# Kernel tuning notes

Measured on AMD Instinct MI355X. Metric: run time of the kernel, lower is better.

The kernel has to match this reference:

```python
import jax, jax.numpy as jnp
import numpy as np

NUM_USERS = 100000
NUM_ITEMS = 50000
EMB_DIM = 64
USER_FEAT = 256
ITEM_FEAT = 256
NUM_EDGES = 1000000
NUM_LAYERS = 4
N = NUM_USERS + NUM_ITEMS


def setup_inputs() -> dict:
    key = jax.random.key(0)
    ks = jax.random.split(key, 8)
    edge_index = jax.random.randint(ks[0], (2, NUM_EDGES), 0, N, dtype=jnp.int64 if jax.config.x64_enabled else jnp.int32).astype(jnp.int32)
    emb_users = jax.random.normal(ks[1], (NUM_USERS, EMB_DIM), dtype=jnp.float32) * 0.1
    emb_items = jax.random.normal(ks[2], (NUM_ITEMS, EMB_DIM), dtype=jnp.float32) * 0.1
    users_features = jax.random.normal(ks[3], (NUM_USERS, USER_FEAT), dtype=jnp.float32)
    items_features = jax.random.normal(ks[4], (NUM_ITEMS, ITEM_FEAT), dtype=jnp.float32)
    # original init is zeros; use small random weights for a non-trivial baseline
    user_proj_w = jax.random.normal(ks[5], (EMB_DIM, USER_FEAT), dtype=jnp.float32) * 0.01
    item_proj_w = jax.random.normal(ks[6], (EMB_DIM, ITEM_FEAT), dtype=jnp.float32) * 0.01
    return {
        "edge_index": edge_index,
        "emb_users": emb_users,
        "emb_items": emb_items,
        "users_features": users_features,
        "items_features": items_features,
        "user_proj_w": user_proj_w,
        "item_proj_w": item_proj_w,
    }


def reference(edge_index, emb_users, emb_items, users_features, items_features, user_proj_w, item_proj_w):
    row, col = edge_index[0], edge_index[1]
    # symmetric GCN normalization without self-loops (PyG LGConv)
    deg = jax.ops.segment_sum(jnp.ones_like(col, dtype=emb_users.dtype), col, num_segments=N)
    dinv = jnp.where(deg > 0, jax.lax.rsqrt(jnp.maximum(deg, 1.0)), 0.0)
    norm = dinv[row] * dinv[col]  # [E]

    x = jnp.concatenate([emb_users, emb_items], axis=0)  # [N, D]
    acc = x
    for _ in range(NUM_LAYERS):
        msgs = x[row] * norm[:, None]                      # [E, D] gather + scale
        x = jax.ops.segment_sum(msgs, col, num_segments=N)  # scatter-add
        acc = acc + x
    # mean over (L+1) layer embeddings, then extra 1/(L+1) factor (faithful to source)
    emb_final = acc / ((NUM_LAYERS + 1) ** 2)

    u_final = emb_final[:NUM_USERS] + users_features @ user_proj_w.T
    i_final = emb_final[NUM_USERS:] + items_features @ item_proj_w.T
    return (u_final, i_final)
```

## Files before the change

### kernel.cpp

```cpp
#include <hip/hip_runtime.h>

#define U_NODES 100000
#define I_NODES 50000
#define N_NODES 150000
#define EMB_D   64
#define FEAT_K  256
#define N_LAYERS 4

typedef __attribute__((ext_vector_type(8))) short short8;
typedef __attribute__((ext_vector_type(4))) float f32x4;

static __device__ __forceinline__ unsigned short f2bf(float f) {
    unsigned u = __builtin_bit_cast(unsigned, f);
    u += 0x7fffu + ((u >> 16) & 1u);
    return (unsigned short)(u >> 16);
}
static __device__ __forceinline__ float bflo(unsigned u) {
    return __builtin_bit_cast(float, u << 16);
}
static __device__ __forceinline__ float bfhi(unsigned u) {
    return __builtin_bit_cast(float, u & 0xffff0000u);
}

__global__ __launch_bounds__(256) void k_count(const int* __restrict__ col,
                                               int* __restrict__ deg, int E) {
    int e = blockIdx.x * 256 + threadIdx.x;
    if (e < E) atomicAdd(&deg[col[e]], 1);
}

__global__ __launch_bounds__(256) void k_dinv(const int* __restrict__ deg,
                                              float* __restrict__ dinv, int n) {
    int i = blockIdx.x * 256 + threadIdx.x;
    if (i < n) {
        int d = deg[i];
        dinv[i] = (d > 0) ? rsqrtf((float)d) : 0.0f;
    }
}

__global__ __launch_bounds__(256) void k_scan_a(const int* __restrict__ deg,
                                                int* __restrict__ rs,
                                                int* __restrict__ bsum, int n) {
    __shared__ int wsum[4];
    int t = threadIdx.x;
    int i = blockIdx.x * 256 + t;
    int v = (i < n) ? deg[i] : 0;
    int x = v;
    #pragma unroll
    for (int off = 1; off < 64; off <<= 1) {
        int y = __shfl_up(x, off, 64);
        if ((t & 63) >= off) x += y;
    }
    if ((t & 63) == 63) wsum[t >> 6] = x;
    __syncthreads();
    int base = 0;
    #pragma unroll
    for (int w = 0; w < 4; ++w) base += (w < (t >> 6)) ? wsum[w] : 0;
    if (i < n) rs[i] = base + x - v;
    if (t == 255) bsum[blockIdx.x] = base + x;
}

__global__ __launch_bounds__(1024) void k_scan_b(int* __restrict__ bs, int nb) {
    __shared__ int wsum[16];
    int t = threadIdx.x;
    int v = (t < nb) ? bs[t] : 0;
    int x = v;
    #pragma unroll
    for (int off = 1; off < 64; off <<= 1) {
        int y = __shfl_up(x, off, 64);
        if ((t & 63) >= off) x += y;
    }
    if ((t & 63) == 63) wsum[t >> 6] = x;
    __syncthreads();
    int base = 0;
    #pragma unroll
    for (int w = 0; w < 16; ++w) base += (w < (t >> 6)) ? wsum[w] : 0;
    if (t < nb) bs[t] = base + x - v;
}

__global__ __launch_bounds__(256) void k_scan_c(int* __restrict__ rs,
                                                const int* __restrict__ bsum,
                                                int* __restrict__ cursor,
                                                int n, int E) {
    int i = blockIdx.x * 256 + threadIdx.x;
    if (i < n) {
        int v = rs[i] + bsum[blockIdx.x];
        rs[i] = v;
        cursor[i] = v;
    }
    if (i == 0) rs[n] = E;
}

__global__ __launch_bounds__(256) void k_fill(const int* __restrict__ row,
                                              const int* __restrict__ col,
                                              const float* __restrict__ dinv,
                                              int* __restrict__ cursor,
                                              int2* __restrict__ csr, int E) {
    int e = blockIdx.x * 256 + threadIdx.x;
    if (e < E) {
        int r = row[e], c = col[e];
        int p = atomicAdd(&cursor[c], 1);
        int2 v;
        v.x = r;
        v.y = __builtin_bit_cast(int, dinv[r] * dinv[c]);
        csr[p] = v;
    }
}

__global__ __launch_bounds__(256) void k_cvtw(const float* __restrict__ wu,
                                              const float* __restrict__ wi,
                                              unsigned short* __restrict__ wub,
                                              unsigned short* __restrict__ wib) {
    int i = blockIdx.x * 256 + threadIdx.x;
    if (i < EMB_D * FEAT_K) wub[i] = f2bf(wu[i]);
    else                    wib[i - EMB_D * FEAT_K] = f2bf(wi[i - EMB_D * FEAT_K]);
}

__global__ __launch_bounds__(256) void k_init(const float4* __restrict__ eu,
                                              const float4* __restrict__ ei,
                                              uint4* __restrict__ x,
                                              int n8u, int n8) {
    int i = blockIdx.x * 256 + threadIdx.x;
    if (i >= n8) return;
    const float4* s = (i < n8u) ? (eu + (size_t)i * 2) : (ei + (size_t)(i - n8u) * 2);
    float4 p0 = s[0], p1 = s[1];
    uint4 r;
    r.x = (unsigned)f2bf(p0.x) | ((unsigned)f2bf(p0.y) << 16);
    r.y = (unsigned)f2bf(p0.z) | ((unsigned)f2bf(p0.w) << 16);
    r.z = (unsigned)f2bf(p1.x) | ((unsigned)f2bf(p1.y) << 16);
    r.w = (unsigned)f2bf(p1.z) | ((unsigned)f2bf(p1.w) << 16);
    x[i] = r;
}

#define ACC8(v_, w_)                       \
    s0 = fmaf(bflo((v_).x), (w_), s0);     \
    s1 = fmaf(bfhi((v_).x), (w_), s1);     \
    s2 = fmaf(bflo((v_).y), (w_), s2);     \
    s3 = fmaf(bfhi((v_).y), (w_), s3);     \
    s4 = fmaf(bflo((v_).z), (w_), s4);     \
    s5 = fmaf(bfhi((v_).z), (w_), s5);     \
    s6 = fmaf(bflo((v_).w), (w_), s6);     \
    s7 = fmaf(bfhi((v_).w), (w_), s7);

#define GATHER4(xsrc_, ep_, em_)                                              \
    {                                                                         \
        int i0_ = (ep_), i1_ = min((ep_) + 1, (em_));                         \
        int i2_ = min((ep_) + 2, (em_)), i3_ = min((ep_) + 3, (em_));         \
        int2 pa_ = csr[i0_], pb_ = csr[i1_], pc_ = csr[i2_], pd_ = csr[i3_];  \
        float wa_ = __builtin_bit_cast(float, pa_.y);                         \
        float wb_ = ((ep_) + 1 <= (em_)) ? __builtin_bit_cast(float, pb_.y) : 0.f; \
        float wc_ = ((ep_) + 2 <= (em_)) ? __builtin_bit_cast(float, pc_.y) : 0.f; \
        float wd_ = ((ep_) + 3 <= (em_)) ? __builtin_bit_cast(float, pd_.y) : 0.f; \
        uint4 va_ = (xsrc_)[(size_t)pa_.x * 8 + lane];                        \
        uint4 vb_ = (xsrc_)[(size_t)pb_.x * 8 + lane];                        \
        uint4 vc_ = (xsrc_)[(size_t)pc_.x * 8 + lane];                        \
        uint4 vd_ = (xsrc_)[(size_t)pd_.x * 8 + lane];                        \
        ACC8(va_, wa_) ACC8(vb_, wb_) ACC8(vc_, wc_) ACC8(vd_, wd_)           \
    }

__global__ __launch_bounds__(256) void k_agg(const uint4* __restrict__ xin,
                                             uint4* __restrict__ xout,
                                             const int* __restrict__ rs,
                                             const int2* __restrict__ csr,
                                             int n_nodes) {
    int idx = blockIdx.x * 256 + threadIdx.x;
    int node = idx >> 3;
    int lane = idx & 7;
    if (node >= n_nodes) return;
    int e0 = rs[node], e1 = rs[node + 1];
    float s0 = 0.f, s1 = 0.f, s2 = 0.f, s3 = 0.f;
    float s4 = 0.f, s5 = 0.f, s6 = 0.f, s7 = 0.f;
    int em = e1 - 1;
    for (int ep = e0; ep < e1; ep += 4) GATHER4(xin, ep, em)
    uint4 r;
    r.x = (unsigned)f2bf(s0) | ((unsigned)f2bf(s1) << 16);
    r.y = (unsigned)f2bf(s2) | ((unsigned)f2bf(s3) << 16);
    r.z = (unsigned)f2bf(s4) | ((unsigned)f2bf(s5) << 16);
    r.w = (unsigned)f2bf(s6) | ((unsigned)f2bf(s7) << 16);
    xout[(size_t)node * 8 + lane] = r;
}

__global__ __launch_bounds__(256) void k_agg4(const uint4* __restrict__ x3,
                                              const uint4* __restrict__ x1,
                                              const uint4* __restrict__ x2,
                                              const float* __restrict__ embU,
                                              const float* __restrict__ embI,
                                              float* __restrict__ outp,
                                              const int* __restrict__ rs,
                                              const int2* __restrict__ csr,
                                              int n_nodes, int U) {
    int idx = blockIdx.x * 256 + threadIdx.x;
    int node = idx >> 3;
    int lane = idx & 7;
    if (node >= n_nodes) return;
    int e0 = rs[node], e1 = rs[node + 1];
    float s0 = 0.f, s1 = 0.f, s2 = 0.f, s3 = 0.f;
    float s4 = 0.f, s5 = 0.f, s6 = 0.f, s7 = 0.f;
    int em = e1 - 1;
    for (int ep = e0; ep < e1; ep += 4) GATHER4(x3, ep, em)
    uint4 v1 = x1[(size_t)node * 8 + lane];
    uint4 v2 = x2[(size_t)node * 8 + lane];
    uint4 v3 = x3[(size_t)node * 8 + lane];
    const float* ebp = (node < U) ? (embU + (size_t)node * EMB_D)
                                  : (embI + (size_t)(node - U) * EMB_D);
    float4 ea = ((const float4*)ebp)[lane * 2];
    float4 eb2 = ((const float4*)ebp)[lane * 2 + 1];
    const float sc = 1.0f / 25.0f;
    float4 o0, o1;
    o0.x = (ea.x  + bflo(v1.x) + bflo(v2.x) + bflo(v3.x) + s0) * sc;
    o0.y = (ea.y  + bfhi(v1.x) + bfhi(v2.x) + bfhi(v3.x) + s1) * sc;
    o0.z = (ea.z  + bflo(v1.y) + bflo(v2.y) + bflo(v3.y) + s2) * sc;
    o0.w = (ea.w  + bfhi(v1.y) + bfhi(v2.y) + bfhi(v3.y) + s3) * sc;
    o1.x = (eb2.x + bflo(v1.z) + bflo(v2.z) + bflo(v3.z) + s4) * sc;
    o1.y = (eb2.y + bfhi(v1.z) + bfhi(v2.z) + bfhi(v3.z) + s5) * sc;
    o1.z = (eb2.z + bflo(v1.w) + bflo(v2.w) + bflo(v3.w) + s6) * sc;
    o1.w = (eb2.w + bfhi(v1.w) + bfhi(v2.w) + bfhi(v3.w) + s7) * sc;
    float4* op = (float4*)(outp + (size_t)node * EMB_D) + lane * 2;
    op[0] = o0;
    op[1] = o1;
}

__global__ __launch_bounds__(256) void k_projm(const float* __restrict__ FU,
                                               const float* __restrict__ FI,
                                               const unsigned short* __restrict__ WUb,
                                               const unsigned short* __restrict__ WIb,
                                               float* __restrict__ out,
                                               int nbU, int U, int I) {
    __shared__ float sA[16 * 256];
    const bool isU = ((int)blockIdx.x < nbU);
    const float* __restrict__ F = isU ? FU : FI;
    const uint4* __restrict__ Wb4 = (const uint4*)(isU ? WUb : WIb);
    float* __restrict__ o = isU ? out : out + (size_t)U * EMB_D;
    const int M = isU ? U : I;
    const int tile = isU ? (int)blockIdx.x : (int)blockIdx.x - nbU;
    const int row0 = tile * 16;
    const int wave = threadIdx.x >> 6;
    const int lane = threadIdx.x & 63;
    const int l15  = lane & 15;
    const int kq   = lane >> 4;

    const uint4* wp = Wb4 + (size_t)(wave * 16 + l15) * 32 + kq;
    uint4 B0 = wp[0],  B1 = wp[4],  B2 = wp[8],  B3 = wp[12];
    uint4 B4 = wp[16], B5 = wp[20], B6 = wp[24], B7 = wp[28];

    #pragma unroll
    for (int j = 0; j < 4; ++j) {
        int r = wave * 4 + j;
        int grow = min(row0 + r, M - 1);
        int sboff = (lane * 16) ^ ((r & 7) << 4);
        const float* src = F + (size_t)grow * FEAT_K + (sboff >> 2);
        __builtin_amdgcn_global_load_lds(
            (const __attribute__((address_space(1))) void*)src,
            (__attribute__((address_space(3))) void*)(sA + r * 256),
            16, 0, 0);
    }
    __syncthreads();

    f32x4 acc = {0.f, 0.f, 0.f, 0.f};
    const char* arow_p = (const char*)(sA + l15 * 256);
    const int sw = (l15 & 7) << 4;

#define CVT2(d_, lo_, hi_) asm("v_cvt_pk_bf16_f32 %0, %1, %2" : "=v"(d_) : "v"(lo_), "v"(hi_))
#define KS(ks_, B_)                                                            \
    {                                                                          \
        int cb = (ks_) * 128 + kq * 32;                                        \
        f32x4 lo = *(const f32x4*)(arow_p + ((cb) ^ sw));                      \
        f32x4 hi = *(const f32x4*)(arow_p + ((cb + 16) ^ sw));                 \
        unsigned p0, p1, p2, p3;                                               \
        CVT2(p0, lo[0], lo[1]); CVT2(p1, lo[2], lo[3]);                        \
        CVT2(p2, hi[0], hi[1]); CVT2(p3, hi[2], hi[3]);                        \
        uint4 up; up.x = p0; up.y = p1; up.z = p2; up.w = p3;                  \
        short8 av = __builtin_bit_cast(short8, up);                            \
        short8 bv = __builtin_bit_cast(short8, B_);                            \
        acc = __builtin_amdgcn_mfma_f32_16x16x32_bf16(av, bv, acc, 0, 0, 0);   \
    }

    KS(0, B0) KS(1, B1) KS(2, B2) KS(3, B3)
    KS(4, B4) KS(5, B5) KS(6, B6) KS(7, B7)
#undef KS
#undef CVT2

    #pragma unroll
    for (int r = 0; r < 4; ++r) {
        int grow = row0 + kq * 4 + r;
        if (grow < M) {
            float* op = o + (size_t)grow * EMB_D + wave * 16 + l15;
            op[0] += acc[r];
        }
    }
}

extern "C" void kernel_launch(void* const* d_in, const int* in_sizes, int n_in,
                              void* d_out, int out_size, void* d_ws, size_t ws_size,
                              hipStream_t stream) {
    const int E = in_sizes[0] / 2;
    const int N = N_NODES, U = U_NODES;

    const int*   edge  = (const int*)d_in[0];
    const float* emb_u = (const float*)d_in[1];
    const float* emb_i = (const float*)d_in[2];
    const float* fu    = (const float*)d_in[3];
    const float* fi    = (const float*)d_in[4];
    const float* wu    = (const float*)d_in[5];
    const float* wi    = (const float*)d_in[6];
    const int* row = edge;
    const int* col = edge + E;

    const int NB  = (N + 255) / 256;
    const int EB  = (E + 255) / 256;
    const int XB8 = ((N * 8) + 255) / 256;

    char* p = (char*)d_ws;
    auto carve = [&](size_t bytes) -> void* {
        void* q = (void*)p;
        p += (bytes + 255) & ~(size_t)255;
        return q;
    };
    float* dinv    = (float*)carve((size_t)N * 4);
    int*   deg     = (int*)  carve((size_t)N * 4);
    int*   rs      = (int*)  carve((size_t)(N + 1) * 4);
    int*   cursor  = (int*)  carve((size_t)N * 4);
    int*   bsum    = (int*)  carve(1024 * 4);
    int2*  csr     = (int2*) carve((size_t)E * 8);
    unsigned short* wub = (unsigned short*)carve((size_t)EMB_D * FEAT_K * 2);
    unsigned short* wib = (unsigned short*)carve((size_t)EMB_D * FEAT_K * 2);
    uint4* x0 = (uint4*)carve((size_t)N * EMB_D * 2);
    uint4* x1 = (uint4*)carve((size_t)N * EMB_D * 2);
    uint4* x2 = (uint4*)carve((size_t)N * EMB_D * 2);
    uint4* x3 = (uint4*)carve((size_t)N * EMB_D * 2);

    float* outp = (float*)d_out;

    hipMemsetAsync(deg, 0, (size_t)N * 4, stream);
    k_count<<<EB, 256, 0, stream>>>(col, deg, E);
    k_dinv<<<NB, 256, 0, stream>>>(deg, dinv, N);
    k_scan_a<<<NB, 256, 0, stream>>>(deg, rs, bsum, N);
    k_scan_b<<<1, 1024, 0, stream>>>(bsum, NB);
    k_scan_c<<<NB, 256, 0, stream>>>(rs, bsum, cursor, N, E);
    k_fill<<<EB, 256, 0, stream>>>(row, col, dinv, cursor, csr, E);
    k_cvtw<<<(2 * EMB_D * FEAT_K) / 256, 256, 0, stream>>>(wu, wi, wub, wib);
    k_init<<<XB8, 256, 0, stream>>>((const float4*)emb_u, (const float4*)emb_i,
                                    x0, U * 8, N * 8);
    k_agg<<<XB8, 256, 0, stream>>>(x0, x1, rs, csr, N);
    k_agg<<<XB8, 256, 0, stream>>>(x1, x2, rs, csr, N);
    k_agg<<<XB8, 256, 0, stream>>>(x2, x3, rs, csr, N);
    k_agg4<<<XB8, 256, 0, stream>>>(x3, x1, x2, emb_u, emb_i, outp, rs, csr, N, U);
    const int nbU = (U + 15) / 16;
    const int nbI = (N - U + 15) / 16;
    k_projm<<<nbU + nbI, 256, 0, stream>>>(fu, fi, wub, wib, outp, nbU, U, N - U);
}
```

Before: 280.8 us.

## Make projection GEMM persistent with double-buffered LDS prefetch; batch k_fill edges

The projection kernel becomes persistent with a fixed grid of 1280 blocks. Each block loops over 16-row tiles and prefetches the next tile's features into a second LDS buffer while the current one runs through MFMA, so global-to-LDS latency overlaps compute. Weights stay in registers and are reloaded only when the loop crosses from the user range into the item range. Separately, k_fill now handles four edges per thread with vectorised int4 loads of row and col, exposing more independent atomics per thread. The cost is manual waitcnt and barrier management, which is fragile, and fewer resident blocks.

```diff
diff --git a/kernel.cpp b/kernel.cpp
--- a/kernel.cpp
+++ b/kernel.cpp
@@ -95,14 +95,30 @@
                                               const float* __restrict__ dinv,
                                               int* __restrict__ cursor,
                                               int2* __restrict__ csr, int E) {
-    int e = blockIdx.x * 256 + threadIdx.x;
-    if (e < E) {
-        int r = row[e], c = col[e];
-        int p = atomicAdd(&cursor[c], 1);
-        int2 v;
-        v.x = r;
-        v.y = __builtin_bit_cast(int, dinv[r] * dinv[c]);
-        csr[p] = v;
+    int base = (blockIdx.x * 256 + threadIdx.x) * 4;
+    if (base >= E) return;
+    if (base + 4 <= E) {
+        int4 c4 = *(const int4*)(col + base);
+        int4 r4 = *(const int4*)(row + base);
+        float na = dinv[r4.x] * dinv[c4.x];
+        float nb = dinv[r4.y] * dinv[c4.y];
+        float nc = dinv[r4.z] * dinv[c4.z];
+        float nd = dinv[r4.w] * dinv[c4.w];
+        int pa = atomicAdd(&cursor[c4.x], 1);
+        int pb = atomicAdd(&cursor[c4.y], 1);
+        int pc = atomicAdd(&cursor[c4.z], 1);
+        int pd = atomicAdd(&cursor[c4.w], 1);
+        int2 va; va.x = r4.x; va.y = __builtin_bit_cast(int, na); csr[pa] = va;
+        int2 vb; vb.x = r4.y; vb.y = __builtin_bit_cast(int, nb); csr[pb] = vb;
+        int2 vc; vc.x = r4.z; vc.y = __builtin_bit_cast(int, nc); csr[pc] = vc;
+        int2 vd; vd.x = r4.w; vd.y = __builtin_bit_cast(int, nd); csr[pd] = vd;
+    } else {
+        for (int e = base; e < E; ++e) {
+            int r = row[e], c = col[e];
+            int p = atomicAdd(&cursor[c], 1);
+            int2 v; v.x = r; v.y = __builtin_bit_cast(int, dinv[r] * dinv[c]);
+            csr[p] = v;
+        }
     }
 }
 
@@ -219,52 +235,88 @@
     op[1] = o1;
 }
 
+#define PROJ_GRID 1280
+
+__device__ __forceinline__ void proj_stage(const float* __restrict__ FU,
+                                           const float* __restrict__ FI,
+                                           int nbU, int U, int I, int t,
+                                           float* dst, int wave, int lane) {
+    bool su = t < nbU;
+    const float* F = su ? FU : FI;
+    int tl = su ? t : t - nbU;
+    int M  = su ? U : I;
+    int r0 = tl * 16;
+    #pragma unroll
+    for (int j = 0; j < 4; ++j) {
+        int r = wave * 4 + j;
+        int g = min(r0 + r, M - 1);
+        int sb = (lane * 16) ^ ((r & 7) << 4);
+        const float* src = F + (size_t)g * FEAT_K + (sb >> 2);
+        __builtin_amdgcn_global_load_lds(
+            (const __attribute__((address_space(1))) void*)src,
+            (__attribute__((address_space(3))) void*)(dst + r * 256),
+            16, 0, 0);
+    }
+}
+
 __global__ __launch_bounds__(256) void k_projm(const float* __restrict__ FU,
                                                const float* __restrict__ FI,
                                                const unsigned short* __restrict__ WUb,
                                                const unsigned short* __restrict__ WIb,
                                                float* __restrict__ out,
-                                               int nbU, int U, int I) {
-    __shared__ float sA[16 * 256];
-    const bool isU = ((int)blockIdx.x < nbU);
-    const float* __restrict__ F = isU ? FU : FI;
-    const uint4* __restrict__ Wb4 = (const uint4*)(isU ? WUb : WIb);
-    float* __restrict__ o = isU ? out : out + (size_t)U * EMB_D;
-    const int M = isU ? U : I;
-    const int tile = isU ? (int)blockIdx.x : (int)blockIdx.x - nbU;
-    const int row0 = tile * 16;
+                                               int nbU, int U, int I, int nT) {
+    __shared__ float sA[2][16 * 256];
     const int wave = threadIdx.x >> 6;
     const int lane = threadIdx.x & 63;
     const int l15  = lane & 15;
     const int kq   = lane >> 4;
-
-    const uint4* wp = Wb4 + (size_t)(wave * 16 + l15) * 32 + kq;
+    const int sw   = (l15 & 7) << 4;
+
+    int t = blockIdx.x;
+    proj_stage(FU, FI, nbU, U, I, t, sA[0], wave, lane);
+    bool curU = (t < nbU);
+    const uint4* wp = (curU ? (const uint4*)WUb : (const uint4*)WIb)
+                      + (size_t)(wave * 16 + l15) * 32 + kq;
     uint4 B0 = wp[0],  B1 = wp[4],  B2 = wp[8],  B3 = wp[12];
     uint4 B4 = wp[16], B5 = wp[20], B6 = wp[24], B7 = wp[28];
 
-    #pragma unroll
-    for (int j = 0; j < 4; ++j) {
-        int r = wave * 4 + j;
-        int grow = min(row0 + r, M - 1);
-        int sboff = (lane * 16) ^ ((r & 7) << 4);
-        const float* src = F + (size_t)grow * FEAT_K + (sboff >> 2);
-        __builtin_amdgcn_global_load_lds(
-            (const __attribute__((address_space(1))) void*)src,
-            (__attribute__((address_space(3))) void*)(sA + r * 256),
-            16, 0, 0);
-    }
-    __syncthreads();
-
-    f32x4 acc = {0.f, 0.f, 0.f, 0.f};
-    const char* arow_p = (const char*)(sA + l15 * 256);
-    const int sw = (l15 & 7) << 4;
+    int buf = 0;
+    for (; t < nT; t += PROJ_GRID) {
+        int tn = t + PROJ_GRID;
+        if (tn < nT) {
+            proj_stage(FU, FI, nbU, U, I, tn, sA[buf ^ 1], wave, lane);
+            asm volatile("s_waitcnt vmcnt(4)" ::: "memory");
+        } else {
+            asm volatile("s_waitcnt vmcnt(0)" ::: "memory");
+        }
+        __builtin_amdgcn_sched_barrier(0);
+        __builtin_amdgcn_s_barrier();
+        __builtin_amdgcn_sched_barrier(0);
+
+        bool u = (t < nbU);
+        if (u != curU) {
+            const uint4* wq = (u ? (const uint4*)WUb : (const uint4*)WIb)
+                              + (size_t)(wave * 16 + l15) * 32 + kq;
+            B0 = wq[0];  B1 = wq[4];  B2 = wq[8];  B3 = wq[12];
+            B4 = wq[16]; B5 = wq[20]; B6 = wq[24]; B7 = wq[28];
+            curU = u;
+        }
+
+        {
+            bool su = u;
+            float* o = su ? out : out + (size_t)U * EMB_D;
+            int tl = su ? t : t - nbU;
+            int M  = su ? U : I;
+            int r0 = tl * 16;
+            f32x4 acc = {0.f, 0.f, 0.f, 0.f};
+            const char* ap = (const char*)(sA[buf] + l15 * 256);
 
 #define CVT2(d_, lo_, hi_) asm("v_cvt_pk_bf16_f32 %0, %1, %2" : "=v"(d_) : "v"(lo_), "v"(hi_))
 #define KS(ks_, B_)                                                            \
     {                                                                          \
         int cb = (ks_) * 128 + kq * 32;                                        \
-        f32x4 lo = *(const f32x4*)(arow_p + ((cb) ^ sw));                      \
-        f32x4 hi = *(const f32x4*)(arow_p + ((cb + 16) ^ sw));                 \
+        f32x4 lo = *(const f32x4*)(ap + ((cb) ^ sw));                          \
+        f32x4 hi = *(const f32x4*)(ap + ((cb + 16) ^ sw));                     \
         unsigned p0, p1, p2, p3;                                               \
         CVT2(p0, lo[0], lo[1]); CVT2(p1, lo[2], lo[3]);                        \
         CVT2(p2, hi[0], hi[1]); CVT2(p3, hi[2], hi[3]);                        \
@@ -273,19 +325,26 @@
         short8 bv = __builtin_bit_cast(short8, B_);                            \
         acc = __builtin_amdgcn_mfma_f32_16x16x32_bf16(av, bv, acc, 0, 0, 0);   \
     }
-
-    KS(0, B0) KS(1, B1) KS(2, B2) KS(3, B3)
-    KS(4, B4) KS(5, B5) KS(6, B6) KS(7, B7)
+            KS(0, B0) KS(1, B1) KS(2, B2) KS(3, B3)
+            KS(4, B4) KS(5, B5) KS(6, B6) KS(7, B7)
 #undef KS
 #undef CVT2
 
-    #pragma unroll
-    for (int r = 0; r < 4; ++r) {
-        int grow = row0 + kq * 4 + r;
-        if (grow < M) {
-            float* op = o + (size_t)grow * EMB_D + wave * 16 + l15;
-            op[0] += acc[r];
+            #pragma unroll
+            for (int r = 0; r < 4; ++r) {
+                int grow = r0 + kq * 4 + r;
+                if (grow < M) {
+                    float* op = o + (size_t)grow * EMB_D + wave * 16 + l15;
+                    op[0] += acc[r];
+                }
+            }
         }
+
+        __builtin_amdgcn_sched_barrier(0);
+        asm volatile("s_waitcnt lgkmcnt(0)" ::: "memory");
+        __builtin_amdgcn_s_barrier();
+        __builtin_amdgcn_sched_barrier(0);
+        buf ^= 1;
     }
 }
 
@@ -336,7 +395,7 @@
     k_scan_a<<<NB, 256, 0, stream>>>(deg, rs, bsum, N);
     k_scan_b<<<1, 1024, 0, stream>>>(bsum, NB);
     k_scan_c<<<NB, 256, 0, stream>>>(rs, bsum, cursor, N, E);
-    k_fill<<<EB, 256, 0, stream>>>(row, col, dinv, cursor, csr, E);
+    k_fill<<<(E / 4 + 255) / 256, 256, 0, stream>>>(row, col, dinv, cursor, csr, E);
     k_cvtw<<<(2 * EMB_D * FEAT_K) / 256, 256, 0, stream>>>(wu, wi, wub, wib);
     k_init<<<XB8, 256, 0, stream>>>((const float4*)emb_u, (const float4*)emb_i,
                                     x0, U * 8, N * 8);
@@ -346,5 +405,6 @@
     k_agg4<<<XB8, 256, 0, stream>>>(x3, x1, x2, emb_u, emb_i, outp, rs, csr, N, U);
     const int nbU = (U + 15) / 16;
     const int nbI = (N - U + 15) / 16;
-    k_projm<<<nbU + nbI, 256, 0, stream>>>(fu, fi, wub, wib, outp, nbU, U, N - U);
-}
+    k_projm<<<PROJ_GRID, 256, 0, stream>>>(fu, fi, wub, wib, outp,
+                                           nbU, U, N - U, nbU + nbI);
+}
```

Result: slower. 311.3 us (+10.9%).
